# Optimization experiments

Measured on AMD Instinct MI355X. Metric: run time of the kernel, lower is better.

Reference implementation:

```python
import jax, jax.numpy as jnp
import numpy as np

B, S, D = 4, 4096, 1024
THETA = 10000.0


def rope(x):
    # x: [..., S, D]; rotates interleaved (even, odd) dim pairs, standard RoPE.
    s, d = x.shape[-2], x.shape[-1]
    pos = jnp.arange(s, dtype=jnp.float32)
    inv_freq = THETA ** (-jnp.arange(0, d, 2, dtype=jnp.float32) / d)  # [d/2]
    ang = pos[:, None] * inv_freq  # [S, d/2]
    c, sn = jnp.cos(ang), jnp.sin(ang)
    e, o = x[..., ::2], x[..., 1::2]
    re = e * c - o * sn
    ro = e * sn + o * c
    return jnp.stack([re, ro], axis=-1).reshape(x.shape)


def setup_inputs() -> dict:
    key = jax.random.key(0)
    k1, k2, k3, k4 = jax.random.split(key, 4)
    scale = 1.0 / np.sqrt(D)
    return {
        "x": jax.random.normal(k1, (B, S, D), dtype=jnp.float32),
        "Wq": jax.random.normal(k2, (D, D), dtype=jnp.float32) * scale,
        "Wk": jax.random.normal(k3, (D, D), dtype=jnp.float32) * scale,
        "Wv": jax.random.normal(k4, (D, D), dtype=jnp.float32) * scale,
    }


def reference(x, Wq, Wk, Wv):
    # QKV projections (Linear with weight [out, in], no bias)
    Q = rope(x @ Wq.T)
    K = rope(x @ Wk.T)
    V = x @ Wv.T
    d = x.shape[-1]
    s = x.shape[-2]
    scores = jnp.einsum('bqd,bkd->bqk', Q, K) / jnp.sqrt(jnp.asarray(d, Q.dtype))
    causal = jnp.tril(jnp.ones((s, s), dtype=bool))
    scores = jnp.where(causal, scores, -jnp.inf)
    attn = jax.nn.softmax(scores, axis=-1)
    return jnp.einsum('bqk,bkd->bqd', attn, V)
```

## Files before the change

kernel.cpp:

```cpp
#include <hip/hip_runtime.h>
#include <math.h>

#define SQ 4096
#define DM 1024
#define NB 4
#define MT (NB*SQ)
#define XN ((size_t)MT*DM)
#define NCVT 19456
#define NTILES 528
#define STILE 16384

typedef __attribute__((ext_vector_type(4))) float f32x4;
typedef __attribute__((ext_vector_type(8))) short s16x8;

__device__ __forceinline__ unsigned short f2bf(float f) {
  union { float f; unsigned int u; } v; v.f = f;
  unsigned int u = v.u;
  u += 0x7fffu + ((u >> 16) & 1u);
  return (unsigned short)(u >> 16);
}

__device__ __forceinline__ float bf2f(unsigned short u) {
  union { unsigned int i; float f; } v; v.i = ((unsigned int)u) << 16;
  return v.f;
}

__device__ __forceinline__ void async16(const void* g, void* l) {
  __builtin_amdgcn_global_load_lds(
      (const __attribute__((address_space(1))) unsigned int*)g,
      (__attribute__((address_space(3))) unsigned int*)l, 16, 0, 0);
}

__global__ __launch_bounds__(256)
void cvt_all(const float* __restrict__ x, const float* __restrict__ Wq,
             const float* __restrict__ Wk, const float* __restrict__ Wv,
             unsigned short* __restrict__ xb, unsigned short* __restrict__ Wb,
             float* __restrict__ l) {
  if (blockIdx.x >= NCVT) {
    int r = (blockIdx.x - NCVT) * 256 + threadIdx.x;
    l[r] = 0.f;
    return;
  }
  size_t i = ((size_t)blockIdx.x * 256 + threadIdx.x) * 4;
  const float* src; unsigned short* dst;
  if (i < XN) { src = x + i; dst = xb + i; }
  else {
    size_t r = i - XN;
    int w = (int)(r >> 20);
    size_t off = r & (((size_t)1 << 20) - 1);
    src = (w == 0 ? Wq : (w == 1 ? Wk : Wv)) + off;
    dst = Wb + r;
  }
  float4 f = *(const float4*)src;
  ushort4 o;
  o.x = f2bf(f.x); o.y = f2bf(f.y); o.z = f2bf(f.z); o.w = f2bf(f.w);
  *(ushort4*)dst = o;
}

template<int LDA, int LDB>
__device__ __forceinline__ void gemm_tile_body(
    const unsigned short* __restrict__ A, const unsigned short* __restrict__ B,
    unsigned short* As, unsigned short* Bs,
    int m0, int n0, int kext, f32x4 acc[4][4]) {
  const int tid = threadIdx.x, lane = tid & 63, wid = tid >> 6;
  const int quad = lane >> 4, l15 = lane & 15;
  const int wm = wid & 1, wn = wid >> 1;

  const int rbase = wid * 32 + (lane >> 3);
  const int kg8   = ((lane & 7) ^ (lane >> 3)) * 8;
  const unsigned short* Ab = A + (size_t)(m0 + rbase) * LDA + kg8;
  const unsigned short* Bb = B + (size_t)(n0 + rbase) * LDB + kg8;
  unsigned short* Asl = As + (wid * 256 + lane) * 8;
  unsigned short* Bsl = Bs + (wid * 256 + lane) * 8;
  const int xorq = (quad ^ (l15 & 7)) * 8;
  const int am = (wm * 64 + l15) * 64 + xorq;
  const int bn = (wn * 64 + l15) * 64 + xorq;

  for (int k0 = 0; k0 < kext; k0 += 64) {
#pragma unroll
    for (int c = 0; c < 4; c++) {
      async16(Ab + (size_t)c * 8 * LDA + k0, Asl + c * 512);
      async16(Bb + (size_t)c * 8 * LDB + k0, Bsl + c * 512);
    }
    asm volatile("s_waitcnt vmcnt(0)" ::: "memory");
    __syncthreads();
#pragma unroll
    for (int ks = 0; ks < 2; ks++) {
      const int ax = am ^ (ks * 32), bx = bn ^ (ks * 32);
      s16x8 af[4], bfr[4];
#pragma unroll
      for (int t = 0; t < 4; t++) {
        af[t]  = *(const s16x8*)(As + ax + t * 1024);
        bfr[t] = *(const s16x8*)(Bs + bx + t * 1024);
      }
#pragma unroll
      for (int tm = 0; tm < 4; tm++)
#pragma unroll
        for (int tn = 0; tn < 4; tn++)
          acc[tm][tn] = __builtin_amdgcn_mfma_f32_16x16x32_bf16(af[tm], bfr[tn], acc[tm][tn], 0, 0, 0);
    }
    __syncthreads();
  }
}

__global__ __launch_bounds__(256, 3)
void proj_all(const unsigned short* __restrict__ A,
              const unsigned short* __restrict__ Wb,
              unsigned short* __restrict__ QKV) {
  __shared__ unsigned short As[128 * 64];
  __shared__ unsigned short Bs[128 * 64];
  const int lane = threadIdx.x & 63, wid = threadIdx.x >> 6;
  const int quad = lane >> 4, l15 = lane & 15;
  const int wm = wid & 1, wn = wid >> 1;
  const int mat = blockIdx.y >> 3;
  const int m0 = blockIdx.x * 128, n0 = (blockIdx.y & 7) * 128;

  f32x4 zero = {0.f, 0.f, 0.f, 0.f};
  f32x4 acc[4][4];
#pragma unroll
  for (int i = 0; i < 4; i++)
#pragma unroll
    for (int j = 0; j < 4; j++) acc[i][j] = zero;

  gemm_tile_body<DM, DM>(A, Wb + (size_t)mat * DM * DM, As, Bs, m0, n0, DM, acc);

  if (mat < 2) {
    unsigned short* C = QKV + (size_t)mat * XN;
    const bool ev = (lane & 1) == 0;
#pragma unroll
    for (int tm = 0; tm < 4; tm++) {
      int rowb = m0 + wm * 64 + tm * 16 + quad * 4;
#pragma unroll
      for (int tn = 0; tn < 4; tn++) {
        int col = n0 + wn * 64 + tn * 16 + l15;
        f32x4 v = acc[tm][tn];
        float invr = exp2f(-(float)(col & ~1) * (13.287712379549449f / 1024.0f)) * 0.15915494309f;
#pragma unroll
        for (int g = 0; g < 4; g++) {
          int row = rowb + g;
          float rev = (float)(row & (SQ - 1)) * invr;
          rev -= floorf(rev);
          float sn, cs;
          __sincosf(rev * 6.283185307179586f, &sn, &cs);
          float part = __shfl_xor(v[g], 1);
          float e = ev ? v[g] : part;
          float o = ev ? part : v[g];
          float re = e * cs - o * sn;
          float ro = e * sn + o * cs;
          if (ev) {
            unsigned int pk = (unsigned int)f2bf(re) | ((unsigned int)f2bf(ro) << 16);
            *(unsigned int*)(C + (size_t)row * DM + col) = pk;
          }
        }
      }
    }
  } else {
    unsigned short* Vt = QKV + (size_t)2 * XN;
#pragma unroll
    for (int tm = 0; tm < 4; tm++) {
      int rowb = m0 + wm * 64 + tm * 16 + quad * 4;
      int b = rowb >> 12;
      int s = rowb & (SQ - 1);
#pragma unroll
      for (int tn = 0; tn < 4; tn++) {
        int col = n0 + wn * 64 + tn * 16 + l15;
        f32x4 v = acc[tm][tn];
        ushort4 o;
        o.x = f2bf(v[0]); o.y = f2bf(v[1]); o.z = f2bf(v[2]); o.w = f2bf(v[3]);
        *(ushort4*)(Vt + (size_t)b * DM * SQ + (size_t)col * SQ + s) = o;
      }
    }
  }
}

__global__ __launch_bounds__(256, 3)
void qk_gemm(const unsigned short* __restrict__ Q, const unsigned short* __restrict__ K,
             unsigned short* __restrict__ S, float* __restrict__ l) {
  __shared__ unsigned short As[128 * 64];
  __shared__ unsigned short Bs[128 * 64];
  const int lane = threadIdx.x & 63, wid = threadIdx.x >> 6;
  const int quad = lane >> 4, l15 = lane & 15;
  const int wm = wid & 1, wn = wid >> 1;

  const int logical = (blockIdx.x & 7) * 264 + (blockIdx.x >> 3);
  const int b = logical / NTILES;
  int t = logical - b * NTILES;
  int mt = (int)((sqrtf(8.f * (float)t + 1.f) - 1.f) * 0.5f);
  while ((mt + 1) * (mt + 2) / 2 <= t) ++mt;
  while (mt * (mt + 1) / 2 > t) --mt;
  int nt = t - mt * (mt + 1) / 2;

  const unsigned short* Qg = Q + (size_t)b * SQ * DM;
  const unsigned short* Kg = K + (size_t)b * SQ * DM;
  unsigned short* Sg = S + (size_t)b * NTILES * STILE + ((size_t)t << 14);
  float* lrow = l + b * SQ;

  f32x4 zero = {0.f, 0.f, 0.f, 0.f};
  f32x4 acc[4][4];
#pragma unroll
  for (int i = 0; i < 4; i++)
#pragma unroll
    for (int j = 0; j < 4; j++) acc[i][j] = zero;

  gemm_tile_body<DM, DM>(Qg, Kg, As, Bs, mt * 128, nt * 128, DM, acc);

  const bool ev = (lane & 1) == 0;
#pragma unroll
  for (int tm = 0; tm < 4; tm++) {
    int lr = wm * 64 + tm * 16 + quad * 4;
    int grow = mt * 128 + lr;
    float rsum[4] = {0.f, 0.f, 0.f, 0.f};
#pragma unroll
    for (int tn = 0; tn < 4; tn++) {
      int lc = wn * 64 + tn * 16 + l15;
      int gcol = nt * 128 + lc;
      f32x4 v = acc[tm][tn];
#pragma unroll
      for (int g = 0; g < 4; g++) {
        float p = (gcol <= grow + g) ? __expf(v[g] * 0.03125f) : 0.f;
        rsum[g] += p;
        float part = __shfl_xor(p, 1);
        if (ev) {
          unsigned int pk = (unsigned int)f2bf(p) | ((unsigned int)f2bf(part) << 16);
          *(unsigned int*)(Sg + (size_t)(lr + g) * 128 + lc) = pk;
        }
      }
    }
#pragma unroll
    for (int g = 0; g < 4; g++) {
      float s = rsum[g];
#pragma unroll
      for (int o = 8; o >= 1; o >>= 1) s += __shfl_xor(s, o);
      if (l15 == 0) atomicAdd(&lrow[grow + g], s);
    }
  }
}

__global__ __launch_bounds__(256, 3)
void pv_pair(const unsigned short* __restrict__ P, const unsigned short* __restrict__ Vt,
             const float* __restrict__ l, float* __restrict__ O) {
  __shared__ unsigned short As[128 * 64];
  __shared__ unsigned short Bs[128 * 64];
  const int lane = threadIdx.x & 63, wid = threadIdx.x >> 6;
  const int quad = lane >> 4, l15 = lane & 15;
  const int wm = wid & 1, wn = wid >> 1;

  const int logical = (blockIdx.x & 7) * 64 + (blockIdx.x >> 3);
  const int b = logical >> 7;
  const int p = (logical >> 3) & 15;
  const int nt = logical & 7;

  const unsigned short* Pg = P + (size_t)b * NTILES * STILE;
  const unsigned short* Vg = Vt + (size_t)b * DM * SQ;
  const float* lg = l + b * SQ;
  float* Og = O + (size_t)b * SQ * DM;
  const int n0 = nt * 128;

  const int rbase = wid * 32 + (lane >> 3);
  const int kg8 = ((lane & 7) ^ (lane >> 3)) * 8;
  const unsigned short* Bb = Vg + (size_t)(n0 + rbase) * SQ + kg8;
  unsigned short* Asl = As + (wid * 256 + lane) * 8;
  unsigned short* Bsl = Bs + (wid * 256 + lane) * 8;
  const int xorq = (quad ^ (l15 & 7)) * 8;
  const int am = (wm * 64 + l15) * 64 + xorq;
  const int bn = (wn * 64 + l15) * 64 + xorq;
  const bool ev = (lane & 1) == 0;

  f32x4 zero = {0.f, 0.f, 0.f, 0.f};
#pragma unroll 1
  for (int half = 0; half < 2; half++) {
    const int mt = half ? (31 - p) : p;
    const int tb = mt * (mt + 1) / 2;
    f32x4 acc[4][4];
#pragma unroll
    for (int i = 0; i < 4; i++)
#pragma unroll
      for (int j = 0; j < 4; j++) acc[i][j] = zero;

    for (int j = 0; j <= mt; ++j) {
      const unsigned short* At = Pg + ((size_t)(tb + j) << 14) + kg8;
      const int kbase = j * 128;
#pragma unroll 1
      for (int ks2 = 0; ks2 < 2; ks2++) {
        const int ko = ks2 * 64;
#pragma unroll
        for (int c = 0; c < 4; c++) {
          async16(At + (size_t)(rbase + 8 * c) * 128 + ko, Asl + c * 512);
          async16(Bb + (size_t)c * 8 * SQ + kbase + ko, Bsl + c * 512);
        }
        asm volatile("s_waitcnt vmcnt(0)" ::: "memory");
        __syncthreads();
#pragma unroll
        for (int ks = 0; ks < 2; ks++) {
          const int ax = am ^ (ks * 32), bx = bn ^ (ks * 32);
          s16x8 af[4], bfr[4];
#pragma unroll
          for (int u = 0; u < 4; u++) {
            af[u]  = *(const s16x8*)(As + ax + u * 1024);
            bfr[u] = *(const s16x8*)(Bs + bx + u * 1024);
          }
#pragma unroll
          for (int tm = 0; tm < 4; tm++)
#pragma unroll
            for (int tn = 0; tn < 4; tn++)
              acc[tm][tn] = __builtin_amdgcn_mfma_f32_16x16x32_bf16(af[tm], bfr[tn], acc[tm][tn], 0, 0, 0);
        }
        __syncthreads();
      }
    }

#pragma unroll
    for (int tm = 0; tm < 4; tm++) {
      int grow = mt * 128 + wm * 64 + tm * 16 + quad * 4;
      float rl[4];
#pragma unroll
      for (int g = 0; g < 4; g++) rl[g] = 1.0f / lg[grow + g];
#pragma unroll
      for (int tn = 0; tn < 4; tn++) {
        int col = n0 + wn * 64 + tn * 16 + l15;
        f32x4 v = acc[tm][tn];
#pragma unroll
        for (int g = 0; g < 4; g++) {
          float val = v[g] * rl[g];
          float part = __shfl_xor(val, 1);
          if (ev) {
            float2 st; st.x = val; st.y = part;
            *(float2*)(Og + (size_t)(grow + g) * DM + col) = st;
          }
        }
      }
    }
  }
}

extern "C" void kernel_launch(void* const* d_in, const int* in_sizes, int n_in,
                              void* d_out, int out_size, void* d_ws, size_t ws_size,
                              hipStream_t stream) {
  const float* x  = (const float*)d_in[0];
  const float* Wq = (const float*)d_in[1];
  const float* Wk = (const float*)d_in[2];
  const float* Wv = (const float*)d_in[3];
  float* out = (float*)d_out;

  unsigned short* Qb  = (unsigned short*)d_ws;
  unsigned short* xb  = Qb + 3 * XN;
  unsigned short* Wb  = xb + XN;
  unsigned short* Sb  = xb;
  float* lfull = (float*)(Sb + (size_t)NB * NTILES * STILE);

  (void)ws_size; (void)in_sizes; (void)n_in; (void)out_size;

  cvt_all<<<NCVT + 64, 256, 0, stream>>>(x, Wq, Wk, Wv, xb, Wb, lfull);

  proj_all<<<dim3(MT / 128, 24), 256, 0, stream>>>(xb, Wb, Qb);

  qk_gemm<<<NB * NTILES, 256, 0, stream>>>(Qb, Qb + XN, Sb, lfull);

  pv_pair<<<512, 256, 0, stream>>>(Sb, Qb + 2 * XN, lfull, out);
}
```

Measured before the change: 417.4 us.

## Rebalance PV GEMM with 64-wide column tiles and bin-packed causal row tiles

Replaces the paired causal row-tile scheme (p with 31-p) in the P·V kernel with a lookup table of 12 bins that group row tiles into roughly equal work. It also halves the output column tile from 128 to 64, so the kernel launches 768 blocks instead of 512. The goal is better load balance and fuller CU occupancy on the triangular workload. In exchange, each block gets fewer MFMAs per P-tile load, so P traffic is re-read twice as often across column tiles.

```diff
diff --git a/kernel.cpp b/kernel.cpp
--- a/kernel.cpp
+++ b/kernel.cpp
@@ -12,6 +12,11 @@
 
 typedef __attribute__((ext_vector_type(4))) float f32x4;
 typedef __attribute__((ext_vector_type(8))) short s16x8;
+
+__device__ const int PV_BIN_START[13] = {0,2,4,6,8,10,12,14,16,18,20,24,32};
+__device__ const int PV_BIN_MT[32] = {31,11, 30,12, 29,13, 28,14, 27,15, 26,16,
+                                      25,17, 24,18, 23,19, 22,20, 21,10,9,0,
+                                      8,7,6,5,4,3,2,1};
 
 __device__ __forceinline__ unsigned short f2bf(float f) {
   union { float f; unsigned int u; } v; v.f = f;
@@ -237,45 +242,45 @@
 }
 
 __global__ __launch_bounds__(256, 3)
-void pv_pair(const unsigned short* __restrict__ P, const unsigned short* __restrict__ Vt,
+void pv_bins(const unsigned short* __restrict__ P, const unsigned short* __restrict__ Vt,
              const float* __restrict__ l, float* __restrict__ O) {
   __shared__ unsigned short As[128 * 64];
-  __shared__ unsigned short Bs[128 * 64];
+  __shared__ unsigned short Bs[64 * 64];
   const int lane = threadIdx.x & 63, wid = threadIdx.x >> 6;
   const int quad = lane >> 4, l15 = lane & 15;
   const int wm = wid & 1, wn = wid >> 1;
 
-  const int logical = (blockIdx.x & 7) * 64 + (blockIdx.x >> 3);
-  const int b = logical >> 7;
-  const int p = (logical >> 3) & 15;
-  const int nt = logical & 7;
+  const int logical = (blockIdx.x & 7) * 96 + (blockIdx.x >> 3);
+  const int nt = logical & 15;
+  const int qb = (logical >> 4) % 12;
+  const int b  = logical / 192;
 
   const unsigned short* Pg = P + (size_t)b * NTILES * STILE;
   const unsigned short* Vg = Vt + (size_t)b * DM * SQ;
   const float* lg = l + b * SQ;
   float* Og = O + (size_t)b * SQ * DM;
-  const int n0 = nt * 128;
-
-  const int rbase = wid * 32 + (lane >> 3);
+  const int n0 = nt * 64;
+
+  const int rbase  = wid * 32 + (lane >> 3);
+  const int rbaseB = wid * 16 + (lane >> 3);
   const int kg8 = ((lane & 7) ^ (lane >> 3)) * 8;
-  const unsigned short* Bb = Vg + (size_t)(n0 + rbase) * SQ + kg8;
+  const unsigned short* Bb = Vg + (size_t)(n0 + rbaseB) * SQ + kg8;
   unsigned short* Asl = As + (wid * 256 + lane) * 8;
-  unsigned short* Bsl = Bs + (wid * 256 + lane) * 8;
+  unsigned short* Bsl = Bs + (wid * 128 + lane) * 8;
   const int xorq = (quad ^ (l15 & 7)) * 8;
   const int am = (wm * 64 + l15) * 64 + xorq;
-  const int bn = (wn * 64 + l15) * 64 + xorq;
+  const int bn = (wn * 32 + l15) * 64 + xorq;
   const bool ev = (lane & 1) == 0;
 
   f32x4 zero = {0.f, 0.f, 0.f, 0.f};
+  const int i0 = PV_BIN_START[qb], i1 = PV_BIN_START[qb + 1];
 #pragma unroll 1
-  for (int half = 0; half < 2; half++) {
-    const int mt = half ? (31 - p) : p;
+  for (int idx = i0; idx < i1; ++idx) {
+    const int mt = PV_BIN_MT[idx];
     const int tb = mt * (mt + 1) / 2;
-    f32x4 acc[4][4];
-#pragma unroll
-    for (int i = 0; i < 4; i++)
-#pragma unroll
-      for (int j = 0; j < 4; j++) acc[i][j] = zero;
+    f32x4 acc[4][2];
+#pragma unroll
+    for (int i = 0; i < 4; i++) { acc[i][0] = zero; acc[i][1] = zero; }
 
     for (int j = 0; j <= mt; ++j) {
       const unsigned short* At = Pg + ((size_t)(tb + j) << 14) + kg8;
@@ -284,25 +289,25 @@
       for (int ks2 = 0; ks2 < 2; ks2++) {
         const int ko = ks2 * 64;
 #pragma unroll
-        for (int c = 0; c < 4; c++) {
+        for (int c = 0; c < 4; c++)
           async16(At + (size_t)(rbase + 8 * c) * 128 + ko, Asl + c * 512);
+#pragma unroll
+        for (int c = 0; c < 2; c++)
           async16(Bb + (size_t)c * 8 * SQ + kbase + ko, Bsl + c * 512);
-        }
         asm volatile("s_waitcnt vmcnt(0)" ::: "memory");
         __syncthreads();
 #pragma unroll
         for (int ks = 0; ks < 2; ks++) {
           const int ax = am ^ (ks * 32), bx = bn ^ (ks * 32);
-          s16x8 af[4], bfr[4];
-#pragma unroll
-          for (int u = 0; u < 4; u++) {
-            af[u]  = *(const s16x8*)(As + ax + u * 1024);
-            bfr[u] = *(const s16x8*)(Bs + bx + u * 1024);
-          }
+          s16x8 af[4], bfr[2];
+#pragma unroll
+          for (int u = 0; u < 4; u++) af[u] = *(const s16x8*)(As + ax + u * 1024);
+#pragma unroll
+          for (int u = 0; u < 2; u++) bfr[u] = *(const s16x8*)(Bs + bx + u * 1024);
 #pragma unroll
           for (int tm = 0; tm < 4; tm++)
 #pragma unroll
-            for (int tn = 0; tn < 4; tn++)
+            for (int tn = 0; tn < 2; tn++)
               acc[tm][tn] = __builtin_amdgcn_mfma_f32_16x16x32_bf16(af[tm], bfr[tn], acc[tm][tn], 0, 0, 0);
         }
         __syncthreads();
@@ -316,8 +321,8 @@
 #pragma unroll
       for (int g = 0; g < 4; g++) rl[g] = 1.0f / lg[grow + g];
 #pragma unroll
-      for (int tn = 0; tn < 4; tn++) {
-        int col = n0 + wn * 64 + tn * 16 + l15;
+      for (int tn = 0; tn < 2; tn++) {
+        int col = n0 + wn * 32 + tn * 16 + l15;
         f32x4 v = acc[tm][tn];
 #pragma unroll
         for (int g = 0; g < 4; g++) {
@@ -356,5 +361,5 @@
 
   qk_gemm<<<NB * NTILES, 256, 0, stream>>>(Qb, Qb + XN, Sb, lfull);
 
-  pv_pair<<<512, 256, 0, stream>>>(Sb, Qb + 2 * XN, lfull, out);
-}
+  pv_bins<<<768, 256, 0, stream>>>(Sb, Qb + 2 * XN, lfull, out);
+}
```

After: 450.1 us. 1.08x slower.

## Share V tile loads across paired short and long row tiles in PV kernel

Applied to the files above, without the earlier changes.

The PV kernel previously ran its two paired row tiles (p and 31-p) one after the other, loading the same V^T column tiles twice for the overlapping K range. It now processes both row tiles in a single K loop with two accumulator sets and two A buffers in shared memory, so each B (V^T) tile is loaded once and used by both. This roughly halves V traffic for the shared range and raises arithmetic intensity per barrier. The cost is double the accumulator registers and more shared memory, so launch bounds drop from 3 to 2 blocks per CU, which lowers occupancy.

```diff
diff --git a/kernel.cpp b/kernel.cpp
--- a/kernel.cpp
+++ b/kernel.cpp
@@ -236,10 +236,11 @@
   }
 }
 
-__global__ __launch_bounds__(256, 3)
+__global__ __launch_bounds__(256, 2)
 void pv_pair(const unsigned short* __restrict__ P, const unsigned short* __restrict__ Vt,
              const float* __restrict__ l, float* __restrict__ O) {
-  __shared__ unsigned short As[128 * 64];
+  __shared__ unsigned short As0[128 * 64];
+  __shared__ unsigned short As1[128 * 64];
   __shared__ unsigned short Bs[128 * 64];
   const int lane = threadIdx.x & 63, wid = threadIdx.x >> 6;
   const int quad = lane >> 4, l15 = lane & 15;
@@ -256,59 +257,83 @@
   float* Og = O + (size_t)b * SQ * DM;
   const int n0 = nt * 128;
 
+  const int mt_s = p, mt_l = 31 - p;
+  const int tb_s = mt_s * (mt_s + 1) / 2;
+  const int tb_l = mt_l * (mt_l + 1) / 2;
+  const int js_max = p + 1, jl_max = 32 - p;
+
   const int rbase = wid * 32 + (lane >> 3);
   const int kg8 = ((lane & 7) ^ (lane >> 3)) * 8;
   const unsigned short* Bb = Vg + (size_t)(n0 + rbase) * SQ + kg8;
-  unsigned short* Asl = As + (wid * 256 + lane) * 8;
-  unsigned short* Bsl = Bs + (wid * 256 + lane) * 8;
+  unsigned short* Asl0 = As0 + (wid * 256 + lane) * 8;
+  unsigned short* Asl1 = As1 + (wid * 256 + lane) * 8;
+  unsigned short* Bsl  = Bs  + (wid * 256 + lane) * 8;
   const int xorq = (quad ^ (l15 & 7)) * 8;
   const int am = (wm * 64 + l15) * 64 + xorq;
   const int bn = (wn * 64 + l15) * 64 + xorq;
   const bool ev = (lane & 1) == 0;
 
   f32x4 zero = {0.f, 0.f, 0.f, 0.f};
+  f32x4 acc_s[4][4], acc_l[4][4];
+#pragma unroll
+  for (int i = 0; i < 4; i++)
+#pragma unroll
+    for (int j = 0; j < 4; j++) { acc_s[i][j] = zero; acc_l[i][j] = zero; }
+
 #pragma unroll 1
+  for (int j = 0; j < jl_max; ++j) {
+    const unsigned short* At_l = Pg + ((size_t)(tb_l + j) << 14) + kg8;
+    const unsigned short* At_s = Pg + ((size_t)(tb_s + j) << 14) + kg8;
+    const bool son = (j < js_max);
+    const int kbase = j * 128;
+#pragma unroll 1
+    for (int ks2 = 0; ks2 < 2; ks2++) {
+      const int ko = ks2 * 64;
+#pragma unroll
+      for (int c = 0; c < 4; c++)
+        async16(At_l + (size_t)(rbase + 8 * c) * 128 + ko, Asl1 + c * 512);
+      if (son) {
+#pragma unroll
+        for (int c = 0; c < 4; c++)
+          async16(At_s + (size_t)(rbase + 8 * c) * 128 + ko, Asl0 + c * 512);
+      }
+#pragma unroll
+      for (int c = 0; c < 4; c++)
+        async16(Bb + (size_t)c * 8 * SQ + kbase + ko, Bsl + c * 512);
+      asm volatile("s_waitcnt vmcnt(0)" ::: "memory");
+      __syncthreads();
+#pragma unroll
+      for (int ks = 0; ks < 2; ks++) {
+        const int ax = am ^ (ks * 32), bx = bn ^ (ks * 32);
+        s16x8 bfr[4];
+#pragma unroll
+        for (int u = 0; u < 4; u++) bfr[u] = *(const s16x8*)(Bs + bx + u * 1024);
+        s16x8 afl[4];
+#pragma unroll
+        for (int u = 0; u < 4; u++) afl[u] = *(const s16x8*)(As1 + ax + u * 1024);
+#pragma unroll
+        for (int tm = 0; tm < 4; tm++)
+#pragma unroll
+          for (int tn = 0; tn < 4; tn++)
+            acc_l[tm][tn] = __builtin_amdgcn_mfma_f32_16x16x32_bf16(afl[tm], bfr[tn], acc_l[tm][tn], 0, 0, 0);
+        if (son) {
+          s16x8 afs[4];
+#pragma unroll
+          for (int u = 0; u < 4; u++) afs[u] = *(const s16x8*)(As0 + ax + u * 1024);
+#pragma unroll
+          for (int tm = 0; tm < 4; tm++)
+#pragma unroll
+            for (int tn = 0; tn < 4; tn++)
+              acc_s[tm][tn] = __builtin_amdgcn_mfma_f32_16x16x32_bf16(afs[tm], bfr[tn], acc_s[tm][tn], 0, 0, 0);
+        }
+      }
+      __syncthreads();
+    }
+  }
+
+#pragma unroll
   for (int half = 0; half < 2; half++) {
-    const int mt = half ? (31 - p) : p;
-    const int tb = mt * (mt + 1) / 2;
-    f32x4 acc[4][4];
-#pragma unroll
-    for (int i = 0; i < 4; i++)
-#pragma unroll
-      for (int j = 0; j < 4; j++) acc[i][j] = zero;
-
-    for (int j = 0; j <= mt; ++j) {
-      const unsigned short* At = Pg + ((size_t)(tb + j) << 14) + kg8;
-      const int kbase = j * 128;
-#pragma unroll 1
-      for (int ks2 = 0; ks2 < 2; ks2++) {
-        const int ko = ks2 * 64;
-#pragma unroll
-        for (int c = 0; c < 4; c++) {
-          async16(At + (size_t)(rbase + 8 * c) * 128 + ko, Asl + c * 512);
-          async16(Bb + (size_t)c * 8 * SQ + kbase + ko, Bsl + c * 512);
-        }
-        asm volatile("s_waitcnt vmcnt(0)" ::: "memory");
-        __syncthreads();
-#pragma unroll
-        for (int ks = 0; ks < 2; ks++) {
-          const int ax = am ^ (ks * 32), bx = bn ^ (ks * 32);
-          s16x8 af[4], bfr[4];
-#pragma unroll
-          for (int u = 0; u < 4; u++) {
-            af[u]  = *(const s16x8*)(As + ax + u * 1024);
-            bfr[u] = *(const s16x8*)(Bs + bx + u * 1024);
-          }
-#pragma unroll
-          for (int tm = 0; tm < 4; tm++)
-#pragma unroll
-            for (int tn = 0; tn < 4; tn++)
-              acc[tm][tn] = __builtin_amdgcn_mfma_f32_16x16x32_bf16(af[tm], bfr[tn], acc[tm][tn], 0, 0, 0);
-        }
-        __syncthreads();
-      }
-    }
-
+    const int mt = half ? mt_l : mt_s;
 #pragma unroll
     for (int tm = 0; tm < 4; tm++) {
       int grow = mt * 128 + wm * 64 + tm * 16 + quad * 4;
@@ -318,7 +343,7 @@
 #pragma unroll
       for (int tn = 0; tn < 4; tn++) {
         int col = n0 + wn * 64 + tn * 16 + l15;
-        f32x4 v = acc[tm][tn];
+        f32x4 v = half ? acc_l[tm][tn] : acc_s[tm][tn];
 #pragma unroll
         for (int g = 0; g < 4; g++) {
           float val = v[g] * rl[g];
```

New measurement: 420.3 us. About the same (+0.7%).
